# Optimization experiments

Hardware: AMD Instinct MI355X
Metric: run time of the kernel (lower is better)

## Reference

```python
import jax, jax.numpy as jnp
import numpy as np

K = 1.0      # spring constant
R0 = 1.0     # equilibrium bond length
EPS = 1e-20  # division guard
NUM_GRAPHS = 64


def setup_inputs() -> dict:
    key = jax.random.key(0)
    k1, k2, k3 = jax.random.split(key, 3)
    N, E = 100000, 3200000
    pos = jax.random.normal(k1, (N, 3), dtype=jnp.float32)
    edge_index = jax.random.randint(k2, (2, E), 0, N, dtype=jnp.int64)
    batch = jnp.sort(jax.random.randint(k3, (N,), 0, NUM_GRAPHS, dtype=jnp.int64))
    return {"pos": pos, "edge_index": edge_index, "batch": batch}


def reference(pos, edge_index, batch):
    i, j = edge_index[0], edge_index[1]
    dr = pos[i] - pos[j]                       # (E, 3)
    d = jnp.linalg.norm(dr, axis=1)            # (E,)
    delta = d - R0
    edge_energy = 0.5 * K * delta ** 2         # (E,)
    energy = jax.ops.segment_sum(edge_energy, batch[i], num_segments=NUM_GRAPHS)
    direction = dr / (d + EPS)[:, None]        # (E, 3)
    force_contrib = (K * delta)[:, None] * direction
    forces = jnp.zeros_like(pos).at[i].add(-force_contrib).at[j].add(force_contrib)
    return energy, forces
```

## Files before the change

### kernel.cpp

```cpp
#include <hip/hip_runtime.h>

#define NUM_GRAPHS 64
#define NSC 160
#define SCN 625
#define SCF 1875
#define XPAD 628
#define SB 512
#define CAP 128
#define SEGSTRIDE (NSC * CAP)
#define PBREC 12800
#define FSCALE 32768.0f
#define FINV   (1.0f / 32768.0f)

__global__ __launch_bounds__(256) void pack_kernel(
    const float* __restrict__ pos, const int* __restrict__ batch,
    float4* __restrict__ pos4, int N)
{
    const int n = blockIdx.x * 256 + threadIdx.x;
    if (n < N) {
        float4 v;
        v.x = pos[3 * n + 0];
        v.y = pos[3 * n + 1];
        v.z = pos[3 * n + 2];
        v.w = __int_as_float(batch[n]);
        pos4[n] = v;
    }
}

__global__ __launch_bounds__(1024, 8) void bin_kernel(
    const int* __restrict__ ei,
    unsigned int* __restrict__ recs,
    int* __restrict__ counts,
    int E, int per_block)
{
    __shared__ unsigned int buf[PBREC];
    __shared__ int hist[NSC];
    __shared__ int csr[NSC];
    __shared__ int cursor[NSC];
    __shared__ int scan_s[NSC];

    const int t = threadIdx.x, b = blockIdx.x;
    const int lane = t & 63, w = t >> 6;
    const int e0 = b * per_block, e1 = min(E, e0 + per_block);

    for (int i = t; i < NSC; i += 1024) hist[i] = 0;
    __syncthreads();

    for (int e = e0 + t; e < e1; e += 1024) {
        const int iv = ei[e], jv = ei[E + e];
        atomicAdd(&hist[iv / SCN], 1);
        atomicAdd(&hist[jv / SCN], 1);
    }
    __syncthreads();

    if (t < NSC) scan_s[t] = hist[t];
    __syncthreads();
    for (int d = 1; d < NSC; d <<= 1) {
        int v = 0;
        if (t < NSC && t >= d) v = scan_s[t - d];
        __syncthreads();
        if (t < NSC) scan_s[t] += v;
        __syncthreads();
    }
    if (t < NSC) {
        const int excl = scan_s[t] - hist[t];
        csr[t] = excl;
        cursor[t] = excl;
    }
    __syncthreads();

    for (int e = e0 + t; e < e1; e += 1024) {
        const int iv = ei[e], jv = ei[E + e];
        const int si = iv / SCN, sj = jv / SCN;
        const int s1 = atomicAdd(&cursor[si], 1);
        buf[s1] = (unsigned int)(iv - si * SCN) | ((unsigned int)jv << 10) | (1u << 27);
        const int s2 = atomicAdd(&cursor[sj], 1);
        buf[s2] = (unsigned int)(jv - sj * SCN) | ((unsigned int)iv << 10);
    }
    __syncthreads();

    unsigned int* dst0 = recs + (size_t)b * NSC * CAP;
    for (int s = w; s < NSC; s += 16) {
        const int base = csr[s];
        const int cnt  = min(hist[s], CAP);
        for (int k = lane; k < cnt; k += 64)
            dst0[s * CAP + k] = buf[base + k];
        if (lane == 0) counts[b * NSC + s] = cnt;
    }
}

template<int G>
__global__ __launch_bounds__(256, 8) void accumulate_kernel(
    const float4* __restrict__ pos4,
    const unsigned int* __restrict__ recs,
    const int* __restrict__ counts,
    float* __restrict__ energy,
    int* __restrict__ xpart,
    unsigned long long* __restrict__ yzpart)
{
    __shared__ float4 slab[SCN];
    __shared__ __align__(16) int facc_x[XPAD];
    __shared__ __align__(16) unsigned long long facc_yz[XPAD];
    __shared__ float ered[8];

    const int t    = threadIdx.x;
    const int lane = t & 63;
    const int w    = t >> 6;
    const int s    = blockIdx.x % NSC;
    const int g    = blockIdx.x / NSC;

    constexpr int SPB   = SB / G;
    constexpr int SPW   = SPB / 4;
    constexpr int NPASS = (SPW + 7) / 8;

    for (int i = t; i < SCN; i += 256) slab[i] = pos4[s * SCN + i];
    for (int i = 4 * t; i < XPAD; i += 1024) {
        int4 z = {0, 0, 0, 0};
        *(int4*)&facc_x[i] = z;
    }
    for (int i = 4 * t; i < 2 * XPAD; i += 1024) {
        int4 z = {0, 0, 0, 0};
        *(int4*)&((int*)facc_yz)[i] = z;
    }
    __syncthreads();

    const int gmin_i = __float_as_int(slab[0].w);
    float e_lo = 0.f, e_hi = 0.f;

    for (int pass = 0; pass < NPASS; ++pass) {
        const int seg0 = g * SPB + w * SPW + pass * 8;
        int v = (lane < 8) ? counts[(seg0 + lane) * NSC + s] : 0;
        #pragma unroll
        for (int d = 1; d < 8; d <<= 1) {
            const int u = __shfl_up(v, d);
            if (lane >= d) v += u;
        }
        const int b0 = __shfl(v, 0), b1 = __shfl(v, 1), b2 = __shfl(v, 2),
                  b3 = __shfl(v, 3), b4 = __shfl(v, 4), b5 = __shfl(v, 5),
                  b6 = __shfl(v, 6);
        const int tot = __shfl(v, 7);
        const unsigned int* bp = recs + ((size_t)seg0 * NSC + s) * CAP;

        for (int base = 0; base < tot; base += 256) {
            unsigned int rec[4];
            bool  val[4];
            int   a[4];
            float4 pb[4];
            #pragma unroll
            for (int u = 0; u < 4; ++u) {
                const int r = base + lane + (u << 6);
                val[u] = r < tot;
                if (val[u]) {
                    const int k = (r >= b0) + (r >= b1) + (r >= b2) + (r >= b3)
                                + (r >= b4) + (r >= b5) + (r >= b6);
                    int prev = 0;
                    prev = (k > 0) ? b0 : prev; prev = (k > 1) ? b1 : prev;
                    prev = (k > 2) ? b2 : prev; prev = (k > 3) ? b3 : prev;
                    prev = (k > 4) ? b4 : prev; prev = (k > 5) ? b5 : prev;
                    prev = (k > 6) ? b6 : prev;
                    rec[u] = bp[(size_t)k * SEGSTRIDE + (r - prev)];
                }
            }
            #pragma unroll
            for (int u = 0; u < 4; ++u) {
                if (val[u]) {
                    a[u]  = (int)(rec[u] & 1023);
                    pb[u] = pos4[(rec[u] >> 10) & 0x1FFFF];
                }
            }
            #pragma unroll
            for (int u = 0; u < 4; ++u) {
                if (val[u]) {
                    const float4 pa = slab[a[u]];
                    const float dx = pa.x - pb[u].x;
                    const float dy = pa.y - pb[u].y;
                    const float dz = pa.z - pb[u].z;
                    const float r2  = fmaxf(dx*dx + dy*dy + dz*dz, 1e-24f);
                    const float inv = __builtin_amdgcn_rsqf(r2);
                    const float sc  = 1.0f - inv;
                    const int xq = __float2int_rn(-sc * dx * FSCALE);
                    const int yq = __float2int_rn(-sc * dy * FSCALE);
                    const int zq = __float2int_rn(-sc * dz * FSCALE);
                    atomicAdd(&facc_x[a[u]], xq);
                    const unsigned long long pk =
                        ((unsigned long long)(unsigned int)zq << 32)
                        + (unsigned long long)(unsigned int)yq;
                    atomicAdd(&facc_yz[a[u]], pk);
                    if (rec[u] >> 27) {
                        const float delta = r2 * inv - 1.0f;
                        const float e = 0.5f * delta * delta;
                        if (__float_as_int(pa.w) == gmin_i) e_lo += e;
                        else                                e_hi += e;
                    }
                }
            }
        }
    }

    #pragma unroll
    for (int d = 32; d > 0; d >>= 1) {
        e_lo += __shfl_down(e_lo, d);
        e_hi += __shfl_down(e_hi, d);
    }
    if (lane == 0) { ered[2 * w] = e_lo; ered[2 * w + 1] = e_hi; }

    __syncthreads();
    int* xdst = xpart + (size_t)(s * G + g) * XPAD;
    unsigned long long* zdst = yzpart + (size_t)(s * G + g) * XPAD;
    for (int i = t; i < SCN; i += 256) xdst[i] = facc_x[i];
    for (int i = t; i < SCN; i += 256) zdst[i] = facc_yz[i];
    if (t == 0)
        atomicAdd(&energy[__float_as_int(slab[0].w)],
                  ered[0] + ered[2] + ered[4] + ered[6]);
    if (t == 1)
        atomicAdd(&energy[__float_as_int(slab[SCN - 1].w)],
                  ered[1] + ered[3] + ered[5] + ered[7]);
}

template<int G>
__global__ __launch_bounds__(256) void reduce_kernel(
    const int* __restrict__ xpart,
    const unsigned long long* __restrict__ yzpart,
    float* __restrict__ forces, int N)
{
    const int n = blockIdx.x * 256 + threadIdx.x;
    if (n >= N) return;
    const int s = n / SCN, a = n - s * SCN;
    int sx = 0, sy = 0, sz = 0;
    #pragma unroll
    for (int g = 0; g < G; ++g) {
        const size_t p = (size_t)(s * G + g) * XPAD + a;
        sx += xpart[p];
        const unsigned long long v = yzpart[p];
        sy += (int)(unsigned int)(v & 0xffffffffull);
        sz += (int)(unsigned int)(v >> 32);
    }
    forces[3 * n + 0] = (float)sx * FINV;
    forces[3 * n + 1] = (float)sy * FINV;
    forces[3 * n + 2] = (float)sz * FINV;
}

extern "C" void kernel_launch(void* const* d_in, const int* in_sizes, int n_in,
                              void* d_out, int out_size, void* d_ws, size_t ws_size,
                              hipStream_t stream) {
    const float* pos   = (const float*)d_in[0];
    const int*   ei    = (const int*)d_in[1];
    const int*   batch = (const int*)d_in[2];

    const int E = in_sizes[1] / 2;
    const int N = in_sizes[0] / 3;

    float* energy = (float*)d_out;
    float* forces = (float*)d_out + NUM_GRAPHS;

    const int per_block = (E + SB - 1) / SB;

    char* w = (char*)d_ws;
    float4* pos4 = (float4*)w;
    size_t off = (size_t)N * 16;
    unsigned int* recs = (unsigned int*)(w + off);
    off += (size_t)SB * NSC * CAP * 4;
    int* counts = (int*)(w + off);
    off += (size_t)SB * NSC * 4;
    int* xpart = (int*)(w + off);
    const size_t xbytes16 = (size_t)NSC * 16 * XPAD * 4;
    const size_t xbytes8  = (size_t)NSC * 8  * XPAD * 4;

    hipMemsetAsync(d_out, 0, NUM_GRAPHS * sizeof(float), stream);

    pack_kernel<<<(N + 255) / 256, 256, 0, stream>>>(pos, batch, pos4, N);

    bin_kernel<<<SB, 1024, 0, stream>>>(ei, recs, counts, E, per_block);

    const size_t need16 = off + xbytes16 + (size_t)NSC * 16 * XPAD * 8;
    if (ws_size >= need16) {
        unsigned long long* yzpart = (unsigned long long*)((char*)xpart + xbytes16);
        accumulate_kernel<16><<<NSC * 16, 256, 0, stream>>>(
            pos4, recs, counts, energy, xpart, yzpart);
        reduce_kernel<16><<<(N + 255) / 256, 256, 0, stream>>>(
            xpart, yzpart, forces, N);
    } else {
        unsigned long long* yzpart = (unsigned long long*)((char*)xpart + xbytes8);
        accumulate_kernel<8><<<NSC * 8, 256, 0, stream>>>(
            pos4, recs, counts, energy, xpart, yzpart);
        reduce_kernel<8><<<(N + 255) / 256, 256, 0, stream>>>(
            xpart, yzpart, forces, N);
    }
}
```

Before: 147.2 us.

## Replace per-block histogram+scan binning with fixed-capacity bins plus overflow path

```diff
diff --git a/kernel.cpp b/kernel.cpp
--- a/kernel.cpp
+++ b/kernel.cpp
@@ -3,12 +3,12 @@
 #define NUM_GRAPHS 64
 #define NSC 160
 #define SCN 625
-#define SCF 1875
 #define XPAD 628
 #define SB 512
 #define CAP 128
+#define CAPL 99
 #define SEGSTRIDE (NSC * CAP)
-#define PBREC 12800
+#define OCAP 65536
 #define FSCALE 32768.0f
 #define FINV   (1.0f / 32768.0f)
 
@@ -31,60 +31,52 @@
     const int* __restrict__ ei,
     unsigned int* __restrict__ recs,
     int* __restrict__ counts,
+    unsigned long long* __restrict__ oflow,
+    int* __restrict__ ocount,
     int E, int per_block)
 {
-    __shared__ unsigned int buf[PBREC];
-    __shared__ int hist[NSC];
-    __shared__ int csr[NSC];
+    __shared__ unsigned int buf[NSC * CAPL];
     __shared__ int cursor[NSC];
-    __shared__ int scan_s[NSC];
 
     const int t = threadIdx.x, b = blockIdx.x;
     const int lane = t & 63, w = t >> 6;
     const int e0 = b * per_block, e1 = min(E, e0 + per_block);
 
-    for (int i = t; i < NSC; i += 1024) hist[i] = 0;
-    __syncthreads();
-
-    for (int e = e0 + t; e < e1; e += 1024) {
-        const int iv = ei[e], jv = ei[E + e];
-        atomicAdd(&hist[iv / SCN], 1);
-        atomicAdd(&hist[jv / SCN], 1);
-    }
-    __syncthreads();
-
-    if (t < NSC) scan_s[t] = hist[t];
-    __syncthreads();
-    for (int d = 1; d < NSC; d <<= 1) {
-        int v = 0;
-        if (t < NSC && t >= d) v = scan_s[t - d];
-        __syncthreads();
-        if (t < NSC) scan_s[t] += v;
-        __syncthreads();
-    }
-    if (t < NSC) {
-        const int excl = scan_s[t] - hist[t];
-        csr[t] = excl;
-        cursor[t] = excl;
-    }
+    for (int i = t; i < NSC; i += 1024) cursor[i] = 0;
     __syncthreads();
 
     for (int e = e0 + t; e < e1; e += 1024) {
         const int iv = ei[e], jv = ei[E + e];
         const int si = iv / SCN, sj = jv / SCN;
         const int s1 = atomicAdd(&cursor[si], 1);
-        buf[s1] = (unsigned int)(iv - si * SCN) | ((unsigned int)jv << 10) | (1u << 27);
+        if (s1 < CAPL) {
+            buf[si * CAPL + s1] = (unsigned int)(iv - si * SCN)
+                                | ((unsigned int)jv << 10) | (1u << 27);
+        } else {
+            const int o = atomicAdd(ocount, 1);
+            if (o < OCAP)
+                oflow[o] = (unsigned long long)(unsigned int)iv
+                         | ((unsigned long long)(unsigned int)jv << 17)
+                         | (1ull << 34);
+        }
         const int s2 = atomicAdd(&cursor[sj], 1);
-        buf[s2] = (unsigned int)(jv - sj * SCN) | ((unsigned int)iv << 10);
+        if (s2 < CAPL) {
+            buf[sj * CAPL + s2] = (unsigned int)(jv - sj * SCN)
+                                | ((unsigned int)iv << 10);
+        } else {
+            const int o = atomicAdd(ocount, 1);
+            if (o < OCAP)
+                oflow[o] = (unsigned long long)(unsigned int)jv
+                         | ((unsigned long long)(unsigned int)iv << 17);
+        }
     }
     __syncthreads();
 
     unsigned int* dst0 = recs + (size_t)b * NSC * CAP;
     for (int s = w; s < NSC; s += 16) {
-        const int base = csr[s];
-        const int cnt  = min(hist[s], CAP);
+        const int cnt = min(cursor[s], CAPL);
         for (int k = lane; k < cnt; k += 64)
-            dst0[s * CAP + k] = buf[base + k];
+            dst0[s * CAP + k] = buf[s * CAPL + k];
         if (lane == 0) counts[b * NSC + s] = cnt;
     }
 }
@@ -240,6 +232,35 @@
     forces[3 * n + 2] = (float)sz * FINV;
 }
 
+__global__ __launch_bounds__(256) void cleanup_kernel(
+    const float4* __restrict__ pos4,
+    const unsigned long long* __restrict__ oflow,
+    const int* __restrict__ ocount,
+    float* __restrict__ energy, float* __restrict__ forces)
+{
+    const int n = min(*ocount, OCAP);
+    for (int i = blockIdx.x * 256 + threadIdx.x; i < n; i += gridDim.x * 256) {
+        const unsigned long long r = oflow[i];
+        const int own = (int)(r & 0x1FFFFull);
+        const int par = (int)((r >> 17) & 0x1FFFFull);
+        const float4 pa = pos4[own];
+        const float4 pb = pos4[par];
+        const float dx = pa.x - pb.x;
+        const float dy = pa.y - pb.y;
+        const float dz = pa.z - pb.z;
+        const float r2  = fmaxf(dx*dx + dy*dy + dz*dz, 1e-24f);
+        const float inv = __builtin_amdgcn_rsqf(r2);
+        const float sc  = 1.0f - inv;
+        atomicAdd(&forces[3 * own + 0], -sc * dx);
+        atomicAdd(&forces[3 * own + 1], -sc * dy);
+        atomicAdd(&forces[3 * own + 2], -sc * dz);
+        if ((r >> 34) & 1ull) {
+            const float delta = r2 * inv - 1.0f;
+            atomicAdd(&energy[__float_as_int(pa.w)], 0.5f * delta * delta);
+        }
+    }
+}
+
 extern "C" void kernel_launch(void* const* d_in, const int* in_sizes, int n_in,
                               void* d_out, int out_size, void* d_ws, size_t ws_size,
                               hipStream_t stream) {
@@ -262,15 +283,21 @@
     off += (size_t)SB * NSC * CAP * 4;
     int* counts = (int*)(w + off);
     off += (size_t)SB * NSC * 4;
+    unsigned long long* oflow = (unsigned long long*)(w + off);
+    off += (size_t)OCAP * 8;
+    int* ocount = (int*)(w + off);
+    off += 256;
     int* xpart = (int*)(w + off);
     const size_t xbytes16 = (size_t)NSC * 16 * XPAD * 4;
     const size_t xbytes8  = (size_t)NSC * 8  * XPAD * 4;
 
     hipMemsetAsync(d_out, 0, NUM_GRAPHS * sizeof(float), stream);
+    hipMemsetAsync(ocount, 0, sizeof(int), stream);
 
     pack_kernel<<<(N + 255) / 256, 256, 0, stream>>>(pos, batch, pos4, N);
 
-    bin_kernel<<<SB, 1024, 0, stream>>>(ei, recs, counts, E, per_block);
+    bin_kernel<<<SB, 1024, 0, stream>>>(ei, recs, counts, oflow, ocount,
+                                        E, per_block);
 
     const size_t need16 = off + xbytes16 + (size_t)NSC * 16 * XPAD * 8;
     if (ws_size >= need16) {
@@ -286,4 +313,6 @@
         reduce_kernel<8><<<(N + 255) / 256, 256, 0, stream>>>(
             xpart, yzpart, forces, N);
     }
-}
+
+    cleanup_kernel<<<16, 256, 0, stream>>>(pos4, oflow, ocount, energy, forces);
+}
```

Result: slower. 171.5 us (+16.5%).
